# Optimization experiments

Measured on AMD Instinct MI355X. Metric: run time of the kernel, lower is better.

Reference implementation:

```python
import jax, jax.numpy as jnp
import numpy as np

HIDDEN = 1024


def setup_inputs() -> dict:
    key = jax.random.key(0)
    kx, kb, kc = jax.random.split(key, 3)
    x = jax.random.normal(kx, (8, 4096, HIDDEN), dtype=jnp.float32)
    logit_a = jnp.zeros((HIDDEN,), dtype=jnp.float32)
    b = jax.random.normal(kb, (HIDDEN,), dtype=jnp.float32) * 0.1
    c = jax.random.normal(kc, (HIDDEN,), dtype=jnp.float32) * 0.1
    d = jnp.zeros((HIDDEN,), dtype=jnp.float32)
    return {"x": x, "logit_a": logit_a, "b": b, "c": c, "d": d}


def reference(x, logit_a, b, c, d):
    # x: (B, T, D); diagonal SSM: s_t = a*s_{t-1} + b*u_t ; y_t = c*s_t + d*u_t
    B, T, D = x.shape
    a = jnp.tanh(logit_a)  # (D,)

    def step(state, u_t):  # state: (B, D), u_t: (B, D)
        state = state * a + u_t * b
        y_t = state * c + u_t * d
        return state, y_t

    xs = jnp.swapaxes(x, 0, 1)  # (T, B, D)
    init = jnp.zeros((B, D), dtype=x.dtype)
    _, ys = jax.lax.scan(step, init, xs)
    return jnp.swapaxes(ys, 0, 1)  # (B, T, D)
```

## Files before the change

### kernel.cpp

```cpp
#include <hip/hip_runtime.h>
#include <math.h>


#define SSM_B 8
#define SSM_T 4096
#define SSM_D 1024
#define SSM_C 128
#define SSM_L 32

typedef float vfloat4 __attribute__((ext_vector_type(4)));

__device__ __forceinline__ float4 f4_fma(float4 a, float4 s, float4 add) {
    return make_float4(fmaf(a.x, s.x, add.x), fmaf(a.y, s.y, add.y),
                       fmaf(a.z, s.z, add.z), fmaf(a.w, s.w, add.w));
}
__device__ __forceinline__ float4 f4_mul(float4 a, float4 b) {
    return make_float4(a.x * b.x, a.y * b.y, a.z * b.z, a.w * b.w);
}
__device__ __forceinline__ void nt_store_f4(float* p, float4 w) {
    vfloat4 v = {w.x, w.y, w.z, w.w};
    __builtin_nontemporal_store(v, (vfloat4*)p);
}

__global__ __launch_bounds__(256) void ssm_pass1(
        const float* __restrict__ x, const float* __restrict__ logit_a,
        const float* __restrict__ bco, float* __restrict__ chunk_end) {
    const int k  = blockIdx.x;
    const int bb = blockIdx.y;
    const int d4 = threadIdx.x * 4;

    float4 la = *(const float4*)(logit_a + d4);
    float4 bv = *(const float4*)(bco + d4);
    float4 a  = make_float4(tanhf(la.x), tanhf(la.y), tanhf(la.z), tanhf(la.w));

    float4 s = make_float4(0.f, 0.f, 0.f, 0.f);
    const float* xp = x + ((size_t)bb * SSM_T + (size_t)k * SSM_L) * SSM_D + d4;
#pragma unroll 8
    for (int t = 0; t < SSM_L; ++t) {
        float4 u = *(const float4*)(xp + (size_t)t * SSM_D);
        s = f4_fma(a, s, f4_mul(bv, u));
    }
    *(float4*)(chunk_end + ((size_t)k * SSM_B + bb) * SSM_D + d4) = s;
}

__global__ __launch_bounds__(256) void ssm_pass2(
        const float* __restrict__ x, const float* __restrict__ logit_a,
        const float* __restrict__ bco, const float* __restrict__ cco,
        const float* __restrict__ dco, const float* __restrict__ chunk_end,
        float* __restrict__ y) {
    const int k  = blockIdx.x;
    const int bb = blockIdx.y;
    const int d4 = threadIdx.x * 4;

    float4 la = *(const float4*)(logit_a + d4);
    float4 bv = *(const float4*)(bco + d4);
    float4 cv = *(const float4*)(cco + d4);
    float4 dv = *(const float4*)(dco + d4);
    float4 a  = make_float4(tanhf(la.x), tanhf(la.y), tanhf(la.z), tanhf(la.w));

    float4 aL = a;
#pragma unroll
    for (int i = 0; i < 5; ++i) aL = f4_mul(aL, aL);

    float4 s = make_float4(0.f, 0.f, 0.f, 0.f);
    for (int j = 0; j < k; ++j) {
        float4 e = *(const float4*)(chunk_end + ((size_t)j * SSM_B + bb) * SSM_D + d4);
        s = f4_fma(aL, s, e);
    }

    const size_t base = ((size_t)bb * SSM_T + (size_t)k * SSM_L) * SSM_D + d4;
    const float* xp = x + base;
    float*       yp = y + base;
#pragma unroll 8
    for (int t = 0; t < SSM_L; ++t) {
        float4 u = *(const float4*)(xp + (size_t)t * SSM_D);
        s = f4_fma(a, s, f4_mul(bv, u));
        float4 w = f4_fma(cv, s, f4_mul(dv, u));
        nt_store_f4(yp + (size_t)t * SSM_D, w);
    }
}

extern "C" void kernel_launch(void* const* d_in, const int* in_sizes, int n_in,
                              void* d_out, int out_size, void* d_ws, size_t ws_size,
                              hipStream_t stream) {
    const float* x   = (const float*)d_in[0];
    const float* la  = (const float*)d_in[1];
    const float* bco = (const float*)d_in[2];
    const float* cco = (const float*)d_in[3];
    const float* dco = (const float*)d_in[4];
    float* y = (float*)d_out;
    float* chunk_end = (float*)d_ws;

    dim3 grid(SSM_C, SSM_B);
    dim3 block(256);
    ssm_pass1<<<grid, block, 0, stream>>>(x, la, bco, chunk_end);
    ssm_pass2<<<grid, block, 0, stream>>>(x, la, bco, cco, dco, chunk_end, y);
}
```

Measured before the change: 275.9 us.

## Add separate chunk-prefix kernel and use nontemporal loads of x in pass2

Replaces the per-block quadratic prefix over previous chunk ends in pass2 with a dedicated scan kernel that writes each chunk's starting state once. pass2 then reads a single precomputed state instead of up to 127 chunk_end entries per block. The x reads in pass2 now use nontemporal loads. This costs an extra launch and a serial 128-step scan running on only 32 blocks.

```diff
diff --git a/kernel.cpp b/kernel.cpp
--- a/kernel.cpp
+++ b/kernel.cpp
@@ -21,6 +21,10 @@
     vfloat4 v = {w.x, w.y, w.z, w.w};
     __builtin_nontemporal_store(v, (vfloat4*)p);
 }
+__device__ __forceinline__ float4 nt_load_f4(const float* p) {
+    vfloat4 v = __builtin_nontemporal_load((const vfloat4*)p);
+    return make_float4(v.x, v.y, v.z, v.w);
+}
 
 __global__ __launch_bounds__(256) void ssm_pass1(
         const float* __restrict__ x, const float* __restrict__ logit_a,
@@ -43,10 +47,34 @@
     *(float4*)(chunk_end + ((size_t)k * SSM_B + bb) * SSM_D + d4) = s;
 }
 
+__global__ __launch_bounds__(256) void ssm_prefix(
+        const float* __restrict__ logit_a,
+        const float* __restrict__ chunk_end,
+        float* __restrict__ chunk_start) {
+    const int tid = blockIdx.x * 256 + threadIdx.x;
+    const int bb  = tid >> 10;
+    const int d   = tid & (SSM_D - 1);
+
+    float a  = tanhf(logit_a[d]);
+    float aL = a;
+#pragma unroll
+    for (int i = 0; i < 5; ++i) aL *= aL;
+
+    float s = 0.f;
+    const size_t stride = (size_t)SSM_B * SSM_D;
+    size_t idx = (size_t)bb * SSM_D + d;
+#pragma unroll 4
+    for (int j = 0; j < SSM_C; ++j) {
+        chunk_start[idx] = s;
+        s = fmaf(aL, s, chunk_end[idx]);
+        idx += stride;
+    }
+}
+
 __global__ __launch_bounds__(256) void ssm_pass2(
         const float* __restrict__ x, const float* __restrict__ logit_a,
         const float* __restrict__ bco, const float* __restrict__ cco,
-        const float* __restrict__ dco, const float* __restrict__ chunk_end,
+        const float* __restrict__ dco, const float* __restrict__ chunk_start,
         float* __restrict__ y) {
     const int k  = blockIdx.x;
     const int bb = blockIdx.y;
@@ -58,22 +86,14 @@
     float4 dv = *(const float4*)(dco + d4);
     float4 a  = make_float4(tanhf(la.x), tanhf(la.y), tanhf(la.z), tanhf(la.w));
 
-    float4 aL = a;
-#pragma unroll
-    for (int i = 0; i < 5; ++i) aL = f4_mul(aL, aL);
-
-    float4 s = make_float4(0.f, 0.f, 0.f, 0.f);
-    for (int j = 0; j < k; ++j) {
-        float4 e = *(const float4*)(chunk_end + ((size_t)j * SSM_B + bb) * SSM_D + d4);
-        s = f4_fma(aL, s, e);
-    }
+    float4 s = *(const float4*)(chunk_start + ((size_t)k * SSM_B + bb) * SSM_D + d4);
 
     const size_t base = ((size_t)bb * SSM_T + (size_t)k * SSM_L) * SSM_D + d4;
     const float* xp = x + base;
     float*       yp = y + base;
 #pragma unroll 8
     for (int t = 0; t < SSM_L; ++t) {
-        float4 u = *(const float4*)(xp + (size_t)t * SSM_D);
+        float4 u = nt_load_f4(xp + (size_t)t * SSM_D);
         s = f4_fma(a, s, f4_mul(bv, u));
         float4 w = f4_fma(cv, s, f4_mul(dv, u));
         nt_store_f4(yp + (size_t)t * SSM_D, w);
@@ -89,10 +109,12 @@
     const float* cco = (const float*)d_in[3];
     const float* dco = (const float*)d_in[4];
     float* y = (float*)d_out;
-    float* chunk_end = (float*)d_ws;
+    float* chunk_end   = (float*)d_ws;
+    float* chunk_start = (float*)d_ws + (size_t)SSM_C * SSM_B * SSM_D;
 
     dim3 grid(SSM_C, SSM_B);
     dim3 block(256);
     ssm_pass1<<<grid, block, 0, stream>>>(x, la, bco, chunk_end);
-    ssm_pass2<<<grid, block, 0, stream>>>(x, la, bco, cco, dco, chunk_end, y);
+    ssm_prefix<<<dim3((SSM_B * SSM_D) / 256), block, 0, stream>>>(la, chunk_end, chunk_start);
+    ssm_pass2<<<grid, block, 0, stream>>>(x, la, bco, cco, dco, chunk_start, y);
 }
```

Measured after the change: 274.6 us. Within noise of the previous version (-0.5%).
